# Performance work log

Hardware: AMD Instinct MI355X
Metric: run time of the kernel (lower is better)

The kernel has to match this reference:

```python
import jax, jax.numpy as jnp
import numpy as np
import math

B, L, HID = 2, 1024, 1536
NH, HD = 24, 64
DSSM = NH * HD            # 1536 (expand = 1)
QKV = 3 * DSSM
DCONV = 2
EPS = 1e-6


def _silu(u):
    return u * jax.nn.sigmoid(u)


def setup_inputs() -> dict:
    key = jax.random.key(0)
    ks = jax.random.split(key, 10)
    x = jax.random.normal(ks[0], (B, L, HID), dtype=jnp.float32)
    w_qkv = jax.random.normal(ks[1], (QKV, HID), dtype=jnp.float32) / math.sqrt(HID)
    conv_w = jax.random.normal(ks[2], (QKV, DCONV), dtype=jnp.float32) * 0.5  # depthwise causal conv, k=2
    w_dt = jax.random.normal(ks[3], (NH, HID), dtype=jnp.float32) * 0.02
    # dt_bias init exactly as in the torch module
    dt = jnp.exp(jax.random.uniform(ks[4], (NH,)) * (math.log(0.1) - math.log(0.001)) + math.log(0.001))
    dt = jnp.clip(dt, 1e-4, None)
    dt_bias = dt + jnp.log(-jnp.expm1(-dt))
    a_log = jnp.log(jax.random.uniform(ks[5], (NH,), minval=1.0, maxval=16.0))
    D = jnp.ones((NH, HD), dtype=jnp.float32)
    w_z = jax.random.normal(ks[6], (DSSM, HID), dtype=jnp.float32) / math.sqrt(HID)
    b_z = jnp.zeros((DSSM,), dtype=jnp.float32)
    rms_w = jnp.ones((DSSM,), dtype=jnp.float32)
    w_o = jax.random.normal(ks[7], (HID, DSSM), dtype=jnp.float32) / math.sqrt(DSSM)
    return dict(x=x, w_qkv=w_qkv, conv_w=conv_w, w_dt=w_dt, dt_bias=dt_bias,
                a_log=a_log, D=D, w_z=w_z, b_z=b_z, rms_w=rms_w, w_o=w_o)


def reference(x, w_qkv, conv_w, w_dt, dt_bias, a_log, D, w_z, b_z, rms_w, w_o):
    # qkv projection  [B,L,3*DSSM]
    qkv = jnp.einsum('blh,qh->blq', x, w_qkv)
    # depthwise causal conv1d (kernel size 2, padding k-1, trimmed to L)
    prev = jnp.pad(qkv, ((0, 0), (1, 0), (0, 0)))[:, :L]
    qkv = _silu(prev * conv_w[:, 0] + qkv * conv_w[:, 1])
    q, k, v = jnp.split(qkv, 3, axis=-1)
    q = q.reshape(B, L, NH, HD)
    k = k.reshape(B, L, NH, HD)
    v = v.reshape(B, L, NH, HD)
    # dt discretization: softplus(dt_proj(x) + dt_bias)   [B,L,NH]
    dt = jax.nn.softplus(jnp.einsum('blh,nh->bln', x, w_dt) + dt_bias)
    A = -jnp.exp(a_log)              # [NH], negative
    dA = dt * A                      # [B,L,NH]
    cs = jnp.transpose(jnp.cumsum(dA, axis=1), (0, 2, 1))   # [B,NH,L]
    diff = cs[:, :, :, None] - cs[:, :, None, :]            # [B,NH,L,L], <=0 on causal part
    causal = jnp.tril(jnp.ones((L, L), dtype=bool))
    decay = jnp.exp(jnp.where(causal, diff, -jnp.inf))      # segment-sum decay matrix
    # quadratic SSD (attention) form of the selective scan
    scores = jnp.einsum('bihd,bjhd->bhij', q, k) * decay
    scores = scores * jnp.transpose(dt, (0, 2, 1))[:, :, None, :]  # dt_j on keys (B-discretization)
    y = jnp.einsum('bhij,bjhd->bihd', scores, v)
    y = y + v * D                    # D skip connection
    y = y.reshape(B, L, DSSM)
    # z gate + RMSNorm + output projection
    z = jnp.einsum('blh,dh->bld', x, w_z) + b_z
    y = y * _silu(z)
    y = y * jax.lax.rsqrt(jnp.mean(y * y, axis=-1, keepdims=True) + EPS) * rms_w
    return jnp.einsum('bld,hd->blh', y, w_o)
```

## Files before the change

kernel.cpp:

```cpp
#include <hip/hip_runtime.h>
#include <hip/hip_bf16.h>
#include <math.h>

#define B_ 2
#define L_ 1024
#define HID_ 1536
#define NH_ 24
#define HD_ 64
#define DSSM_ 1536
#define QKV_ 4608
#define M_ 2048

typedef __attribute__((ext_vector_type(8))) short short8;
typedef __attribute__((ext_vector_type(4))) short short4e;
typedef __attribute__((ext_vector_type(4))) float floatx4;

__device__ __forceinline__ void gload_lds16(const short* g, short* l)
{
    __builtin_amdgcn_global_load_lds(
        (const __attribute__((address_space(1))) void*)g,
        (__attribute__((address_space(3))) void*)l,
        16, 0, 0);
}

__device__ __forceinline__ float bfs2f(short s)
{
    unsigned u = ((unsigned)(unsigned short)s) << 16;
    float f; __builtin_memcpy(&f, &u, 4); return f;
}
__device__ __forceinline__ short f2bfs(float f)
{
    __hip_bfloat16 h = __float2bfloat16(f);
    short s; __builtin_memcpy(&s, &h, 2); return s;
}

__device__ const int pIt[15] = {0,1,2,3,3,4,4,5,5,6,6,6,7,7,7};
__device__ const int pJ0[15] = {0,0,0,0,6,0,6,0,6,0,6,12,0,6,12};
__device__ const int pSl[15] = {0,0,0,0,1,0,1,0,1,0,1,2,0,1,2};

#define CN0 (M_ * HID_)
#define CN1 (QKV_ * HID_)
#define CN2 (DSSM_ * HID_)
#define CN3 (HID_ * DSSM_)
__global__ void cast_w_kernel(
    const float* __restrict__ wq,
    const float* __restrict__ wz, const float* __restrict__ wo,
    __hip_bfloat16* __restrict__ wcat,
    __hip_bfloat16* __restrict__ wob)
{
    int i = (blockIdx.x * 256 + threadIdx.x) * 4;
    const float* src; __hip_bfloat16* dst; int off;
    if (i < CN1)             { src = wq; dst = wcat;       off = i; }
    else if (i < CN1 + CN2)  { src = wz; dst = wcat + CN1; off = i - CN1; }
    else                     { src = wo; dst = wob;        off = i - CN1 - CN2; }
    float4 f = *reinterpret_cast<const float4*>(src + off);
    dst[off]     = __float2bfloat16(f.x);
    dst[off + 1] = __float2bfloat16(f.y);
    dst[off + 2] = __float2bfloat16(f.z);
    dst[off + 3] = __float2bfloat16(f.w);
}

#define MFMA_ __builtin_amdgcn_mfma_f32_16x16x32_bf16
#define BAR_() __builtin_amdgcn_s_barrier()
#define SCHED_ __builtin_amdgcn_sched_barrier(0)

#define CSTR 200

__global__ __launch_bounds__(256, 2) void gemm_qkvz_128(
    const __hip_bfloat16* __restrict__ A,
    const __hip_bfloat16* __restrict__ Bm,
    __hip_bfloat16* __restrict__ qkv_out,
    float* __restrict__ z_out,
    const float* __restrict__ b_z)
{
    extern __shared__ short lds[];
    const int K  = HID_;
    const int NT = K / 64;
    const int tid   = threadIdx.x;
    const int lane  = tid & 63;
    const int wave  = tid >> 6;
    const int col16 = lane & 15;
    const int quad  = lane >> 4;
    const int wm = wave >> 1;
    const int wn = wave & 1;
    const int rowblk = blockIdx.y * 128;
    const int colblk = blockIdx.x * 192;

    const short* Ap = reinterpret_cast<const short*>(A);
    const short* Bp = reinterpret_cast<const short*>(Bm);

    const int o  = tid * 16;
    const int s  = o ^ (((o >> 7) & 7) << 4);
    const int sr = s >> 7;
    const int sc = (s & 127) >> 1;

    const int mask = (col16 & 7) << 4;
    const int e0 = ((quad * 16)      ^ mask) >> 1;
    const int e1 = ((64 + quad * 16) ^ mask) >> 1;
    const int arow = (wm * 64 + col16) * 64;
    const int brow = (wn * 96 + col16) * 64;

    floatx4 acc[4][6] = {};

    auto STAGE_ALL = [&](int c, int t) {
        const short* ga = Ap + (size_t)(rowblk + sr) * K + t * 64 + sc;
        short* da = &lds[c * 8192 + tid * 8];
#pragma unroll
        for (int u = 0; u < 4; ++u)
            gload_lds16(ga + (size_t)(u * 32) * K, da + u * 2048);
        const short* gb = Bp + (size_t)(colblk + sr) * K + t * 64 + sc;
        short* db = &lds[16384 + c * 12288 + tid * 8];
#pragma unroll
        for (int u = 0; u < 6; ++u)
            gload_lds16(gb + (size_t)(u * 32) * K, db + u * 2048);
    };

    STAGE_ALL(0, 0);
    asm volatile("s_waitcnt vmcnt(0)" ::: "memory");
    SCHED_;
    BAR_();

    for (int t = 0; t < NT; ++t) {
        const int cur = t & 1;
        if (t + 1 < NT) STAGE_ALL(cur ^ 1, t + 1);

        const int Ab = cur * 8192;
        const int Bb = 16384 + cur * 12288;
        short8 af0[4], af1[4], bf0[6], bf1[6];
#pragma unroll
        for (int m = 0; m < 4; ++m) {
            af0[m] = *reinterpret_cast<const short8*>(&lds[Ab + arow + m * 1024 + e0]);
            af1[m] = *reinterpret_cast<const short8*>(&lds[Ab + arow + m * 1024 + e1]);
        }
#pragma unroll
        for (int n = 0; n < 6; ++n) {
            bf0[n] = *reinterpret_cast<const short8*>(&lds[Bb + brow + n * 1024 + e0]);
            bf1[n] = *reinterpret_cast<const short8*>(&lds[Bb + brow + n * 1024 + e1]);
        }
        asm volatile("s_waitcnt lgkmcnt(0)" ::: "memory");
        SCHED_;

        __builtin_amdgcn_s_setprio(1);
#pragma unroll
        for (int m = 0; m < 4; ++m)
#pragma unroll
            for (int n = 0; n < 6; ++n) {
                acc[m][n] = MFMA_(af0[m], bf0[n], acc[m][n], 0, 0, 0);
                acc[m][n] = MFMA_(af1[m], bf1[n], acc[m][n], 0, 0, 0);
            }
        __builtin_amdgcn_s_setprio(0);

        asm volatile("s_waitcnt vmcnt(0)" ::: "memory");
        SCHED_;
        BAR_();
    }

    if (blockIdx.x < 24) {
        const int rb = wm * 64 + quad * 4;
        const int cb = wn * 96 + col16;
#pragma unroll
        for (int m = 0; m < 4; ++m)
#pragma unroll
            for (int n = 0; n < 6; ++n)
#pragma unroll
                for (int r = 0; r < 4; ++r)
                    lds[(rb + m * 16 + r) * CSTR + cb + n * 16] =
                        f2bfs(acc[m][n][r]);
        __syncthreads();
        const int row = tid >> 1;
        const int seg = tid & 1;
        const short* srcp = &lds[row * CSTR + seg * 96];
        short* dstp = reinterpret_cast<short*>(qkv_out)
                    + (size_t)(rowblk + row) * QKV_ + colblk + seg * 96;
#pragma unroll
        for (int j = 0; j < 12; ++j)
            *reinterpret_cast<short8*>(dstp + j * 8) =
                *reinterpret_cast<const short8*>(srcp + j * 8);
    } else {
        const int row0  = rowblk + wm * 64;
        const int col0g = colblk + wn * 96 - QKV_;
#pragma unroll
        for (int m = 0; m < 4; ++m)
#pragma unroll
            for (int n = 0; n < 6; ++n)
#pragma unroll
                for (int r = 0; r < 4; ++r) {
                    int row = row0 + m * 16 + quad * 4 + r;
                    int col = col0g + n * 16 + col16;
                    z_out[(size_t)row * DSSM_ + col] = acc[m][n][r] + b_z[col];
                }
    }
}

template<int OUTMODE>
__global__ __launch_bounds__(256) void gemm_nt(
    const __hip_bfloat16* __restrict__ A,
    const __hip_bfloat16* __restrict__ Bm,
    void* __restrict__ Cv,
    const float* __restrict__ bias,
    int M, int N, int K)
{
    const int lane  = threadIdx.x & 63;
    const int wave  = threadIdx.x >> 6;
    const int col16 = lane & 15;
    const int quad  = lane >> 4;
    const int wr    = wave >> 1;
    const int wc    = wave & 1;
    const int rowblk = blockIdx.y * 128;
    const int colblk = blockIdx.x * 128;

    const short* Ap = reinterpret_cast<const short*>(A);
    const short* Bp = reinterpret_cast<const short*>(Bm);

    __shared__ alignas(16) short As[128 * 32];
    __shared__ alignas(16) short Bs[128 * 32];

    const int srow = lane >> 2;
    const int scol = (lane & 3) * 8;

    floatx4 acc[4][4] = {};

    for (int k0 = 0; k0 < K; k0 += 32) {
#pragma unroll
        for (int s2 = 0; s2 < 2; ++s2) {
            const int seg = wave * 2 + s2;
            gload_lds16(Ap + (size_t)(rowblk + seg * 16 + srow) * K + k0 + scol,
                        &As[seg * 512]);
            gload_lds16(Bp + (size_t)(colblk + seg * 16 + srow) * K + k0 + scol,
                        &Bs[seg * 512]);
        }
        __syncthreads();

        short8 af[4], bf[4];
#pragma unroll
        for (int t = 0; t < 4; ++t) {
            af[t] = *reinterpret_cast<const short8*>(
                &As[(wr * 64 + t * 16 + col16) * 32 + quad * 8]);
            bf[t] = *reinterpret_cast<const short8*>(
                &Bs[(wc * 64 + t * 16 + col16) * 32 + quad * 8]);
        }
#pragma unroll
        for (int mt = 0; mt < 4; ++mt)
#pragma unroll
            for (int nt = 0; nt < 4; ++nt)
                acc[mt][nt] = __builtin_amdgcn_mfma_f32_16x16x32_bf16(
                    af[mt], bf[nt], acc[mt][nt], 0, 0, 0);
        __syncthreads();
    }

    const int row0 = rowblk + wr * 64;
    const int col0 = colblk + wc * 64;
#pragma unroll
    for (int mt = 0; mt < 4; ++mt) {
#pragma unroll
        for (int nt = 0; nt < 4; ++nt) {
#pragma unroll
            for (int r = 0; r < 4; ++r) {
                int row = row0 + mt * 16 + quad * 4 + r;
                int col = col0 + nt * 16 + col16;
                float v = acc[mt][nt][r];
                if (OUTMODE == 1) v += bias[col];
                if (OUTMODE == 2)
                    ((__hip_bfloat16*)Cv)[(size_t)row * N + col] = __float2bfloat16(v);
                else
                    ((float*)Cv)[(size_t)row * N + col] = v;
            }
        }
    }
}

__global__ void conv_silu_kernel(
    const __hip_bfloat16* __restrict__ raw,
    const float* __restrict__ conv_w,
    __hip_bfloat16* __restrict__ q,
    __hip_bfloat16* __restrict__ k,
    __hip_bfloat16* __restrict__ v)
{
    int idx8 = blockIdx.x * 256 + threadIdx.x;
    int c8 = (idx8 % (QKV_ / 8)) * 8;
    int ml = idx8 / (QKV_ / 8);
    int l  = ml % L_;
    int b  = ml / L_;

    const short* base = reinterpret_cast<const short*>(raw) + (size_t)ml * QKV_ + c8;
    short8 curv = *reinterpret_cast<const short8*>(base);
    short8 prevv = {};
    if (l > 0) prevv = *reinterpret_cast<const short8*>(base - QKV_);

    float4 w0 = *reinterpret_cast<const float4*>(conv_w + c8 * 2);
    float4 w1 = *reinterpret_cast<const float4*>(conv_w + c8 * 2 + 4);
    float4 w2 = *reinterpret_cast<const float4*>(conv_w + c8 * 2 + 8);
    float4 w3 = *reinterpret_cast<const float4*>(conv_w + c8 * 2 + 12);
    const float wa[16] = {w0.x, w0.y, w0.z, w0.w, w1.x, w1.y, w1.z, w1.w,
                          w2.x, w2.y, w2.z, w2.w, w3.x, w3.y, w3.z, w3.w};

    short8 outv;
#pragma unroll
    for (int j = 0; j < 8; ++j) {
        float u = bfs2f(prevv[j]) * wa[2 * j] + bfs2f(curv[j]) * wa[2 * j + 1];
        u = fmaxf(u, -80.f);
        outv[j] = f2bfs(u / (1.f + __expf(-u)));
    }

    int part = c8 / DSSM_;
    int cc   = c8 % DSSM_;
    int nh   = cc >> 6;
    int d    = cc & 63;
    __hip_bfloat16* dst = (part == 0) ? q : ((part == 1) ? k : v);
    *reinterpret_cast<short8*>(
        reinterpret_cast<short*>(dst) + (((size_t)b * NH_ + nh) * L_ + l) * HD_ + d)
        = outv;
}

__global__ __launch_bounds__(256) void dtproj_kernel(
    const float* __restrict__ x,
    const float* __restrict__ w_dt,
    const float* __restrict__ dt_bias,
    const float* __restrict__ a_log,
    float* __restrict__ dt,
    float* __restrict__ dA,
    __hip_bfloat16* __restrict__ xb)
{
    const int tid  = threadIdx.x;
    const int wave = tid >> 6;
    const int lane = tid & 63;
    const int m0   = blockIdx.x * 8 + wave * 2;

    float4 xa[2][6];
#pragma unroll
    for (int rr = 0; rr < 2; ++rr)
#pragma unroll
        for (int j = 0; j < 6; ++j)
            xa[rr][j] = *reinterpret_cast<const float4*>(
                x + (size_t)(m0 + rr) * HID_ + lane * 4 + j * 256);

    short* xbp = reinterpret_cast<short*>(xb);
#pragma unroll
    for (int rr = 0; rr < 2; ++rr)
#pragma unroll
        for (int j = 0; j < 6; ++j) {
            short4e ov;
            ov[0] = f2bfs(xa[rr][j].x); ov[1] = f2bfs(xa[rr][j].y);
            ov[2] = f2bfs(xa[rr][j].z); ov[3] = f2bfs(xa[rr][j].w);
            *reinterpret_cast<short4e*>(
                xbp + (size_t)(m0 + rr) * HID_ + lane * 4 + j * 256) = ov;
        }

    float acc0[NH_], acc1[NH_];
#pragma unroll
    for (int n = 0; n < NH_; ++n) {
        float s0 = 0.f, s1 = 0.f;
#pragma unroll
        for (int j = 0; j < 6; ++j) {
            float4 w = *reinterpret_cast<const float4*>(
                w_dt + (size_t)n * HID_ + lane * 4 + j * 256);
            s0 += xa[0][j].x * w.x + xa[0][j].y * w.y
                + xa[0][j].z * w.z + xa[0][j].w * w.w;
            s1 += xa[1][j].x * w.x + xa[1][j].y * w.y
                + xa[1][j].z * w.z + xa[1][j].w * w.w;
        }
        acc0[n] = s0;
        acc1[n] = s1;
    }

#pragma unroll
    for (int off = 32; off; off >>= 1) {
#pragma unroll
        for (int n = 0; n < NH_; ++n) {
            acc0[n] += __shfl_xor(acc0[n], off, 64);
            acc1[n] += __shfl_xor(acc1[n], off, 64);
        }
    }

    if (lane < NH_) {
        const int n = lane;
        float bias = dt_bias[n];
        float Aval = -__expf(a_log[n]);
        float v0 = acc0[n] + bias;
        float v1 = acc1[n] + bias;
        v0 = (v0 > 20.f) ? v0 : log1pf(__expf(v0));
        v1 = (v1 > 20.f) ? v1 : log1pf(__expf(v1));
        int b0 = m0 / L_, l0 = m0 % L_;
        size_t o0 = ((size_t)b0 * NH_ + n) * L_ + l0;
        dt[o0]     = v0;
        dA[o0]     = v0 * Aval;
        dt[o0 + 1] = v1;
        dA[o0 + 1] = v1 * Aval;
    }
}

__global__ void cumsum_kernel(const float* __restrict__ dA, float* __restrict__ cs)
{
    int bnh  = blockIdx.x;
    int lane = threadIdx.x;
    const float* src = dA + (size_t)bnh * L_;
    float* dst       = cs + (size_t)bnh * L_;

    float loc[16];
    float run = 0.f;
#pragma unroll
    for (int t = 0; t < 16; ++t) { run += src[lane * 16 + t]; loc[t] = run; }
    float tot = run;
    float sc = tot;
#pragma unroll
    for (int off = 1; off < 64; off <<= 1) {
        float o = __shfl_up(sc, off, 64);
        if (lane >= off) sc += o;
    }
    float offset = sc - tot;
#pragma unroll
    for (int t = 0; t < 16; ++t) dst[lane * 16 + t] = loc[t] + offset;
}

__global__ __launch_bounds__(256) void vdt_transpose_kernel(
    const __hip_bfloat16* __restrict__ v,
    const float* __restrict__ dt,
    __hip_bfloat16* __restrict__ vt)
{
    const int lt0 = blockIdx.x * 64;
    const int bnh = blockIdx.z * NH_ + blockIdx.y;
    const int tid = threadIdx.x;

    __shared__ short T[64][72];

    {
        int row = tid >> 2;
        int cc  = (tid & 3) * 16;
        const short* sp = reinterpret_cast<const short*>(v)
                        + ((size_t)bnh * L_ + lt0 + row) * HD_ + cc;
        float dtr = dt[(size_t)bnh * L_ + lt0 + row];
        short8 a = *reinterpret_cast<const short8*>(sp);
        short8 b = *reinterpret_cast<const short8*>(sp + 8);
#pragma unroll
        for (int j = 0; j < 8; ++j) {
            T[row][cc + j]     = f2bfs(bfs2f(a[j]) * dtr);
            T[row][cc + 8 + j] = f2bfs(bfs2f(b[j]) * dtr);
        }
    }
    __syncthreads();
    {
        int d  = tid >> 2;
        int lc = (tid & 3) * 16;
        short8 o0, o1;
#pragma unroll
        for (int j = 0; j < 8; ++j) {
            o0[j] = T[lc + j][d];
            o1[j] = T[lc + 8 + j][d];
        }
        short* dst = reinterpret_cast<short*>(vt)
                   + ((size_t)bnh * HD_ + d) * L_ + lt0 + lc;
        *reinterpret_cast<short8*>(dst)     = o0;
        *reinterpret_cast<short8*>(dst + 8) = o1;
    }
}

__global__ __launch_bounds__(256) void attn_kernel(
    const __hip_bfloat16* __restrict__ q,
    const __hip_bfloat16* __restrict__ k,
    const __hip_bfloat16* __restrict__ vt,
    const float* __restrict__ cs,
    float* __restrict__ p0,
    float* __restrict__ p1,
    float* __restrict__ p2)
{
    const int bid  = blockIdx.x;
    const int xcd  = bid & 7;
    const int tq   = bid >> 3;
    const int g    = (tq / 15) * 8 + xcd;
    const int pidx = tq % 15;
    const int it   = pIt[pidx];
    const int sl   = pSl[pidx];
    const int jt_beg = pJ0[pidx];
    const int b    = g / NH_;
    const int nh   = g % NH_;
    const int tid  = threadIdx.x;
    const int lane = tid & 63;
    const int wave = tid >> 6;
    const int col  = lane & 15;
    const int quad = lane >> 4;
    const int bnh  = b * NH_ + nh;
    const int iw0  = it * 128 + wave * 16;
    const int iw1  = iw0 + 64;

    float* pout = (sl == 0) ? p0 : ((sl == 1) ? p1 : p2);

    const short* qp  = reinterpret_cast<const short*>(q);
    const short* kp  = reinterpret_cast<const short*>(k);
    const short* vtp = reinterpret_cast<const short*>(vt);

    __shared__ alignas(16) short Ks[4096];
    __shared__ alignas(16) short Ps[4 * 2 * 16 * 72];
    __shared__ float Cj[384];

    const int jbase = jt_beg * 64;
    const int jlim  = min(384, L_ - jbase);
    if (tid < (jlim >> 2))
        *reinterpret_cast<float4*>(&Cj[tid * 4]) =
            *reinterpret_cast<const float4*>(cs + (size_t)bnh * L_ + jbase + tid * 4);

    const short* qrow0 = qp + ((size_t)bnh * L_ + iw0 + col) * HD_;
    const short* qrow1 = qp + ((size_t)bnh * L_ + iw1 + col) * HD_;
    short8 aq0_0 = *reinterpret_cast<const short8*>(qrow0 + quad * 8);
    short8 aq0_1 = *reinterpret_cast<const short8*>(qrow0 + 32 + quad * 8);
    short8 aq1_0 = *reinterpret_cast<const short8*>(qrow1 + quad * 8);
    short8 aq1_1 = *reinterpret_cast<const short8*>(qrow1 + 32 + quad * 8);

    float csr0[4], csr1[4];
#pragma unroll
    for (int r = 0; r < 4; ++r) {
        csr0[r] = cs[(size_t)bnh * L_ + iw0 + quad * 4 + r];
        csr1[r] = cs[(size_t)bnh * L_ + iw1 + quad * 4 + r];
    }

    auto STAGE_K = [&](int jt2) {
        const short* gk = kp + ((size_t)bnh * L_ + jt2 * 64 + wave * 16 + (lane >> 2)) * HD_
                        + (lane & 3) * 8;
        gload_lds16(gk,      &Ks[wave * 512 + lane * 8]);
        gload_lds16(gk + 32, &Ks[2048 + wave * 512 + lane * 8]);
    };

    const int jt_end = min(jt_beg + 5, 2 * it + 1);

    STAGE_K(jt_beg);

    floatx4 accO0[4] = {};
    floatx4 accO1[4] = {};

    for (int jt = jt_beg; jt <= jt_end; ++jt) {
        const int j0 = jt * 64;

        asm volatile("s_waitcnt vmcnt(0)" ::: "memory");
        SCHED_;
        __syncthreads();

        short8 bv[2][4];
#pragma unroll
        for (int c = 0; c < 2; ++c) {
            if (j0 + c * 32 <= iw1 + 15) {
#pragma unroll
                for (int nt = 0; nt < 4; ++nt)
                    bv[c][nt] = *reinterpret_cast<const short8*>(
                        vtp + ((size_t)bnh * HD_ + nt * 16 + col) * L_
                            + j0 + c * 32 + quad * 8);
            }
        }

#pragma unroll
        for (int s = 0; s < 4; ++s) {
            int jsub = j0 + s * 16;
            short8 bk0 = *reinterpret_cast<const short8*>(
                &Ks[(s * 16 + col) * 32 + quad * 8]);
            short8 bk1 = *reinterpret_cast<const short8*>(
                &Ks[2048 + (s * 16 + col) * 32 + quad * 8]);
            int j = jsub + col;
            float csj = Cj[j - jbase];

            if (jsub <= iw0 + 15) {
                floatx4 sc = {};
                sc = __builtin_amdgcn_mfma_f32_16x16x32_bf16(aq0_0, bk0, sc, 0, 0, 0);
                sc = __builtin_amdgcn_mfma_f32_16x16x32_bf16(aq0_1, bk1, sc, 0, 0, 0);
#pragma unroll
                for (int r = 0; r < 4; ++r) {
                    int i = iw0 + quad * 4 + r;
                    float e = (j <= i) ? __expf(csr0[r] - csj) : 0.f;
                    Ps[wave * 2304 + (quad * 4 + r) * 72 + s * 16 + col] =
                        f2bfs(sc[r] * e);
                }
            } else if (j0 + (s >> 1) * 32 <= iw0 + 15) {
#pragma unroll
                for (int r = 0; r < 4; ++r)
                    Ps[wave * 2304 + (quad * 4 + r) * 72 + s * 16 + col] = 0;
            }

            if (jsub <= iw1 + 15) {
                floatx4 sc = {};
                sc = __builtin_amdgcn_mfma_f32_16x16x32_bf16(aq1_0, bk0, sc, 0, 0, 0);
                sc = __builtin_amdgcn_mfma_f32_16x16x32_bf16(aq1_1, bk1, sc, 0, 0, 0);
#pragma unroll
                for (int r = 0; r < 4; ++r) {
                    int i = iw1 + quad * 4 + r;
                    float e = (j <= i) ? __expf(csr1[r] - csj) : 0.f;
                    Ps[wave * 2304 + 1152 + (quad * 4 + r) * 72 + s * 16 + col] =
                        f2bfs(sc[r] * e);
                }
            } else if (j0 + (s >> 1) * 32 <= iw1 + 15) {
#pragma unroll
                for (int r = 0; r < 4; ++r)
                    Ps[wave * 2304 + 1152 + (quad * 4 + r) * 72 + s * 16 + col] = 0;
            }
        }

#pragma unroll
        for (int c = 0; c < 2; ++c) {
            if (j0 + c * 32 <= iw0 + 15) {
                short8 pa = *reinterpret_cast<const short8*>(
                    &Ps[wave * 2304 + col * 72 + c * 32 + quad * 8]);
#pragma unroll
                for (int nt = 0; nt < 4; ++nt)
                    accO0[nt] = __builtin_amdgcn_mfma_f32_16x16x32_bf16(
                        pa, bv[c][nt], accO0[nt], 0, 0, 0);
            }
            if (j0 + c * 32 <= iw1 + 15) {
                short8 pa = *reinterpret_cast<const short8*>(
                    &Ps[wave * 2304 + 1152 + col * 72 + c * 32 + quad * 8]);
#pragma unroll
                for (int nt = 0; nt < 4; ++nt)
                    accO1[nt] = __builtin_amdgcn_mfma_f32_16x16x32_bf16(
                        pa, bv[c][nt], accO1[nt], 0, 0, 0);
            }
        }

        __syncthreads();
        if (jt < jt_end) STAGE_K(jt + 1);
    }

#pragma unroll
    for (int nt = 0; nt < 4; ++nt) {
#pragma unroll
        for (int r = 0; r < 4; ++r) {
            int dv = nt * 16 + col;
            int i0 = iw0 + quad * 4 + r;
            int i1 = iw1 + quad * 4 + r;
            pout[((size_t)b * L_ + i0) * DSSM_ + nh * HD_ + dv] = accO0[nt][r];
            pout[((size_t)b * L_ + i1) * DSSM_ + nh * HD_ + dv] = accO1[nt][r];
        }
    }
}

__global__ __launch_bounds__(256) void gate_rms_kernel(
    const float* __restrict__ p0,
    const float* __restrict__ p1,
    const float* __restrict__ p2,
    const float* __restrict__ z,
    const __hip_bfloat16* __restrict__ v,
    const float* __restrict__ Dm,
    const float* __restrict__ rms_w,
    __hip_bfloat16* __restrict__ yn)
{
    int m   = blockIdx.x;
    int b   = m / L_;
    int l   = m % L_;
    int tid = threadIdx.x;
    size_t base = (size_t)m * DSSM_;
    const bool has1 = (l >= 384);
    const bool has2 = (l >= 768);

    floatx4 acc4[2] = {};
    float ss = 0.f;
#pragma unroll
    for (int t = 0; t < 2; ++t) {
        int i4 = t * 256 + tid;
        if (i4 < DSSM_ / 4) {
            int c  = i4 * 4;
            int nh = c >> 6, d = c & 63;
            floatx4 p = *reinterpret_cast<const floatx4*>(p0 + base + c);
            if (has1) p += *reinterpret_cast<const floatx4*>(p1 + base + c);
            if (has2) p += *reinterpret_cast<const floatx4*>(p2 + base + c);
            floatx4 dm = *reinterpret_cast<const floatx4*>(Dm + c);
            floatx4 zz = *reinterpret_cast<const floatx4*>(z + base + c);
            short4e vv = *reinterpret_cast<const short4e*>(
                reinterpret_cast<const short*>(v)
                + (((size_t)b * NH_ + nh) * L_ + l) * HD_ + d);
            floatx4 g;
#pragma unroll
            for (int j = 0; j < 4; ++j) {
                float yv = p[j] + bfs2f(vv[j]) * dm[j];
                float zv = fmaxf(zz[j], -80.f);
                float gv = yv * (zv / (1.f + __expf(-zv)));
                ss += gv * gv;
                g[j] = gv;
            }
            acc4[t] = g;
        }
    }
#pragma unroll
    for (int off = 32; off; off >>= 1) ss += __shfl_xor(ss, off, 64);
    __shared__ float red[4];
    if ((tid & 63) == 0) red[tid >> 6] = ss;
    __syncthreads();
    ss = red[0] + red[1] + red[2] + red[3];
    float r = rsqrtf(ss / (float)DSSM_ + 1e-6f);
#pragma unroll
    for (int t = 0; t < 2; ++t) {
        int i4 = t * 256 + tid;
        if (i4 < DSSM_ / 4) {
            int c = i4 * 4;
            floatx4 rw = *reinterpret_cast<const floatx4*>(rms_w + c);
            short4e o;
#pragma unroll
            for (int j = 0; j < 4; ++j)
                o[j] = f2bfs(acc4[t][j] * r * rw[j]);
            *reinterpret_cast<short4e*>(
                reinterpret_cast<short*>(yn) + base + c) = o;
        }
    }
}

extern "C" void kernel_launch(void* const* d_in, const int* in_sizes, int n_in,
                              void* d_out, int out_size, void* d_ws, size_t ws_size,
                              hipStream_t stream)
{
    const float* x       = (const float*)d_in[0];
    const float* w_qkv   = (const float*)d_in[1];
    const float* conv_w  = (const float*)d_in[2];
    const float* w_dt    = (const float*)d_in[3];
    const float* dt_bias = (const float*)d_in[4];
    const float* a_log   = (const float*)d_in[5];
    const float* Dm      = (const float*)d_in[6];
    const float* w_z     = (const float*)d_in[7];
    const float* b_z     = (const float*)d_in[8];
    const float* rms_w   = (const float*)d_in[9];
    const float* w_o     = (const float*)d_in[10];
    float* out = (float*)d_out;

    char* ws = (char*)d_ws;

    __hip_bfloat16* xb    = (__hip_bfloat16*)(ws);
    __hip_bfloat16* wob   = (__hip_bfloat16*)(ws + 6291456);
    float*          zbuf  = (float*)(ws + 11010048);
    __hip_bfloat16* wcat  = (__hip_bfloat16*)(ws + 23592960);
    __hip_bfloat16* qkvb  = (__hip_bfloat16*)(ws + 42467328);
    __hip_bfloat16* qb    = (__hip_bfloat16*)(ws + 61341696);
    __hip_bfloat16* kb    = (__hip_bfloat16*)(ws + 67633152);
    __hip_bfloat16* vb    = (__hip_bfloat16*)(ws + 73924608);
    float* dt   = (float*)(ws + 80216064);
    float* dA   = (float*)(ws + 80412672);
    float* cs   = (float*)(ws + 80609280);
    __hip_bfloat16* vtb = (__hip_bfloat16*)(ws);
    __hip_bfloat16* yn  = (__hip_bfloat16*)(ws);
    float* p0 = (float*)(ws + 23592960);
    float* p1 = (float*)(ws + 36175872);
    float* p2 = (float*)(ws + 48758784);

    static bool attr_set = false;
    if (!attr_set) {
        (void)hipFuncSetAttribute(reinterpret_cast<const void*>(gemm_qkvz_128),
                                  hipFuncAttributeMaxDynamicSharedMemorySize,
                                  81920);
        attr_set = true;
    }

    cast_w_kernel<<<(CN1 + CN2 + CN3) / 1024, 256, 0, stream>>>(
        w_qkv, w_z, w_o, wcat, wob);

    dtproj_kernel<<<M_ / 8, 256, 0, stream>>>(
        x, w_dt, dt_bias, a_log, dt, dA, xb);

    cumsum_kernel<<<B_ * NH_, 64, 0, stream>>>(dA, cs);

    gemm_qkvz_128<<<dim3((QKV_ + DSSM_) / 192, M_ / 128), 256, 81920, stream>>>(
        xb, wcat, qkvb, zbuf, b_z);

    conv_silu_kernel<<<(B_ * L_ * QKV_ / 8) / 256, 256, 0, stream>>>(
        qkvb, conv_w, qb, kb, vb);

    vdt_transpose_kernel<<<dim3(L_ / 64, NH_, B_), 256, 0, stream>>>(vb, dt, vtb);

    attn_kernel<<<720, 256, 0, stream>>>(
        qb, kb, vtb, cs, p0, p1, p2);

    gate_rms_kernel<<<M_, 256, 0, stream>>>(p0, p1, p2, zbuf, vb, Dm, rms_w, yn);

    gemm_nt<0><<<dim3(HID_ / 128, M_ / 128), 256, 0, stream>>>(
        yn, wob, (void*)out, nullptr, M_, HID_, DSSM_);
}
```

Measured before the change: 261.8 us.

## Fuse weight cast into dtproj, conv with v transpose, cumsum into attention

Merges the weight-cast kernel into the dt-projection kernel, combines the conv+SiLU kernel with the v*dt transpose kernel so v is computed straight from the raw qkv, and moves the per-head cumsum into each attention block using a block-wide scan over dA. This cuts three kernel launches and the intermediate round trips through global memory for cs and for v. In exchange every attention block now recomputes a full 1024-length prefix sum and pays an extra barrier, which adds a little redundant work per block.

```diff
diff --git a/kernel.cpp b/kernel.cpp
--- a/kernel.cpp
+++ b/kernel.cpp
@@ -38,289 +38,42 @@
 __device__ const int pJ0[15] = {0,0,0,0,6,0,6,0,6,0,6,12,0,6,12};
 __device__ const int pSl[15] = {0,0,0,0,1,0,1,0,1,0,1,2,0,1,2};
 
-#define CN0 (M_ * HID_)
 #define CN1 (QKV_ * HID_)
 #define CN2 (DSSM_ * HID_)
 #define CN3 (HID_ * DSSM_)
-__global__ void cast_w_kernel(
-    const float* __restrict__ wq,
-    const float* __restrict__ wz, const float* __restrict__ wo,
-    __hip_bfloat16* __restrict__ wcat,
-    __hip_bfloat16* __restrict__ wob)
-{
-    int i = (blockIdx.x * 256 + threadIdx.x) * 4;
-    const float* src; __hip_bfloat16* dst; int off;
-    if (i < CN1)             { src = wq; dst = wcat;       off = i; }
-    else if (i < CN1 + CN2)  { src = wz; dst = wcat + CN1; off = i - CN1; }
-    else                     { src = wo; dst = wob;        off = i - CN1 - CN2; }
-    float4 f = *reinterpret_cast<const float4*>(src + off);
-    dst[off]     = __float2bfloat16(f.x);
-    dst[off + 1] = __float2bfloat16(f.y);
-    dst[off + 2] = __float2bfloat16(f.z);
-    dst[off + 3] = __float2bfloat16(f.w);
-}
 
 #define MFMA_ __builtin_amdgcn_mfma_f32_16x16x32_bf16
 #define BAR_() __builtin_amdgcn_s_barrier()
 #define SCHED_ __builtin_amdgcn_sched_barrier(0)
 
-#define CSTR 200
-
-__global__ __launch_bounds__(256, 2) void gemm_qkvz_128(
-    const __hip_bfloat16* __restrict__ A,
-    const __hip_bfloat16* __restrict__ Bm,
-    __hip_bfloat16* __restrict__ qkv_out,
-    float* __restrict__ z_out,
-    const float* __restrict__ b_z)
-{
-    extern __shared__ short lds[];
-    const int K  = HID_;
-    const int NT = K / 64;
-    const int tid   = threadIdx.x;
-    const int lane  = tid & 63;
-    const int wave  = tid >> 6;
-    const int col16 = lane & 15;
-    const int quad  = lane >> 4;
-    const int wm = wave >> 1;
-    const int wn = wave & 1;
-    const int rowblk = blockIdx.y * 128;
-    const int colblk = blockIdx.x * 192;
-
-    const short* Ap = reinterpret_cast<const short*>(A);
-    const short* Bp = reinterpret_cast<const short*>(Bm);
-
-    const int o  = tid * 16;
-    const int s  = o ^ (((o >> 7) & 7) << 4);
-    const int sr = s >> 7;
-    const int sc = (s & 127) >> 1;
-
-    const int mask = (col16 & 7) << 4;
-    const int e0 = ((quad * 16)      ^ mask) >> 1;
-    const int e1 = ((64 + quad * 16) ^ mask) >> 1;
-    const int arow = (wm * 64 + col16) * 64;
-    const int brow = (wn * 96 + col16) * 64;
-
-    floatx4 acc[4][6] = {};
-
-    auto STAGE_ALL = [&](int c, int t) {
-        const short* ga = Ap + (size_t)(rowblk + sr) * K + t * 64 + sc;
-        short* da = &lds[c * 8192 + tid * 8];
-#pragma unroll
-        for (int u = 0; u < 4; ++u)
-            gload_lds16(ga + (size_t)(u * 32) * K, da + u * 2048);
-        const short* gb = Bp + (size_t)(colblk + sr) * K + t * 64 + sc;
-        short* db = &lds[16384 + c * 12288 + tid * 8];
-#pragma unroll
-        for (int u = 0; u < 6; ++u)
-            gload_lds16(gb + (size_t)(u * 32) * K, db + u * 2048);
-    };
-
-    STAGE_ALL(0, 0);
-    asm volatile("s_waitcnt vmcnt(0)" ::: "memory");
-    SCHED_;
-    BAR_();
-
-    for (int t = 0; t < NT; ++t) {
-        const int cur = t & 1;
-        if (t + 1 < NT) STAGE_ALL(cur ^ 1, t + 1);
-
-        const int Ab = cur * 8192;
-        const int Bb = 16384 + cur * 12288;
-        short8 af0[4], af1[4], bf0[6], bf1[6];
-#pragma unroll
-        for (int m = 0; m < 4; ++m) {
-            af0[m] = *reinterpret_cast<const short8*>(&lds[Ab + arow + m * 1024 + e0]);
-            af1[m] = *reinterpret_cast<const short8*>(&lds[Ab + arow + m * 1024 + e1]);
-        }
-#pragma unroll
-        for (int n = 0; n < 6; ++n) {
-            bf0[n] = *reinterpret_cast<const short8*>(&lds[Bb + brow + n * 1024 + e0]);
-            bf1[n] = *reinterpret_cast<const short8*>(&lds[Bb + brow + n * 1024 + e1]);
-        }
-        asm volatile("s_waitcnt lgkmcnt(0)" ::: "memory");
-        SCHED_;
-
-        __builtin_amdgcn_s_setprio(1);
-#pragma unroll
-        for (int m = 0; m < 4; ++m)
-#pragma unroll
-            for (int n = 0; n < 6; ++n) {
-                acc[m][n] = MFMA_(af0[m], bf0[n], acc[m][n], 0, 0, 0);
-                acc[m][n] = MFMA_(af1[m], bf1[n], acc[m][n], 0, 0, 0);
-            }
-        __builtin_amdgcn_s_setprio(0);
-
-        asm volatile("s_waitcnt vmcnt(0)" ::: "memory");
-        SCHED_;
-        BAR_();
-    }
-
-    if (blockIdx.x < 24) {
-        const int rb = wm * 64 + quad * 4;
-        const int cb = wn * 96 + col16;
-#pragma unroll
-        for (int m = 0; m < 4; ++m)
-#pragma unroll
-            for (int n = 0; n < 6; ++n)
-#pragma unroll
-                for (int r = 0; r < 4; ++r)
-                    lds[(rb + m * 16 + r) * CSTR + cb + n * 16] =
-                        f2bfs(acc[m][n][r]);
-        __syncthreads();
-        const int row = tid >> 1;
-        const int seg = tid & 1;
-        const short* srcp = &lds[row * CSTR + seg * 96];
-        short* dstp = reinterpret_cast<short*>(qkv_out)
-                    + (size_t)(rowblk + row) * QKV_ + colblk + seg * 96;
-#pragma unroll
-        for (int j = 0; j < 12; ++j)
-            *reinterpret_cast<short8*>(dstp + j * 8) =
-                *reinterpret_cast<const short8*>(srcp + j * 8);
-    } else {
-        const int row0  = rowblk + wm * 64;
-        const int col0g = colblk + wn * 96 - QKV_;
-#pragma unroll
-        for (int m = 0; m < 4; ++m)
-#pragma unroll
-            for (int n = 0; n < 6; ++n)
-#pragma unroll
-                for (int r = 0; r < 4; ++r) {
-                    int row = row0 + m * 16 + quad * 4 + r;
-                    int col = col0g + n * 16 + col16;
-                    z_out[(size_t)row * DSSM_ + col] = acc[m][n][r] + b_z[col];
-                }
-    }
-}
-
-template<int OUTMODE>
-__global__ __launch_bounds__(256) void gemm_nt(
-    const __hip_bfloat16* __restrict__ A,
-    const __hip_bfloat16* __restrict__ Bm,
-    void* __restrict__ Cv,
-    const float* __restrict__ bias,
-    int M, int N, int K)
-{
-    const int lane  = threadIdx.x & 63;
-    const int wave  = threadIdx.x >> 6;
-    const int col16 = lane & 15;
-    const int quad  = lane >> 4;
-    const int wr    = wave >> 1;
-    const int wc    = wave & 1;
-    const int rowblk = blockIdx.y * 128;
-    const int colblk = blockIdx.x * 128;
-
-    const short* Ap = reinterpret_cast<const short*>(A);
-    const short* Bp = reinterpret_cast<const short*>(Bm);
-
-    __shared__ alignas(16) short As[128 * 32];
-    __shared__ alignas(16) short Bs[128 * 32];
-
-    const int srow = lane >> 2;
-    const int scol = (lane & 3) * 8;
-
-    floatx4 acc[4][4] = {};
-
-    for (int k0 = 0; k0 < K; k0 += 32) {
-#pragma unroll
-        for (int s2 = 0; s2 < 2; ++s2) {
-            const int seg = wave * 2 + s2;
-            gload_lds16(Ap + (size_t)(rowblk + seg * 16 + srow) * K + k0 + scol,
-                        &As[seg * 512]);
-            gload_lds16(Bp + (size_t)(colblk + seg * 16 + srow) * K + k0 + scol,
-                        &Bs[seg * 512]);
-        }
-        __syncthreads();
-
-        short8 af[4], bf[4];
-#pragma unroll
-        for (int t = 0; t < 4; ++t) {
-            af[t] = *reinterpret_cast<const short8*>(
-                &As[(wr * 64 + t * 16 + col16) * 32 + quad * 8]);
-            bf[t] = *reinterpret_cast<const short8*>(
-                &Bs[(wc * 64 + t * 16 + col16) * 32 + quad * 8]);
-        }
-#pragma unroll
-        for (int mt = 0; mt < 4; ++mt)
-#pragma unroll
-            for (int nt = 0; nt < 4; ++nt)
-                acc[mt][nt] = __builtin_amdgcn_mfma_f32_16x16x32_bf16(
-                    af[mt], bf[nt], acc[mt][nt], 0, 0, 0);
-        __syncthreads();
-    }
-
-    const int row0 = rowblk + wr * 64;
-    const int col0 = colblk + wc * 64;
-#pragma unroll
-    for (int mt = 0; mt < 4; ++mt) {
-#pragma unroll
-        for (int nt = 0; nt < 4; ++nt) {
-#pragma unroll
-            for (int r = 0; r < 4; ++r) {
-                int row = row0 + mt * 16 + quad * 4 + r;
-                int col = col0 + nt * 16 + col16;
-                float v = acc[mt][nt][r];
-                if (OUTMODE == 1) v += bias[col];
-                if (OUTMODE == 2)
-                    ((__hip_bfloat16*)Cv)[(size_t)row * N + col] = __float2bfloat16(v);
-                else
-                    ((float*)Cv)[(size_t)row * N + col] = v;
-            }
-        }
-    }
-}
-
-__global__ void conv_silu_kernel(
-    const __hip_bfloat16* __restrict__ raw,
-    const float* __restrict__ conv_w,
-    __hip_bfloat16* __restrict__ q,
-    __hip_bfloat16* __restrict__ k,
-    __hip_bfloat16* __restrict__ v)
-{
-    int idx8 = blockIdx.x * 256 + threadIdx.x;
-    int c8 = (idx8 % (QKV_ / 8)) * 8;
-    int ml = idx8 / (QKV_ / 8);
-    int l  = ml % L_;
-    int b  = ml / L_;
-
-    const short* base = reinterpret_cast<const short*>(raw) + (size_t)ml * QKV_ + c8;
-    short8 curv = *reinterpret_cast<const short8*>(base);
-    short8 prevv = {};
-    if (l > 0) prevv = *reinterpret_cast<const short8*>(base - QKV_);
-
-    float4 w0 = *reinterpret_cast<const float4*>(conv_w + c8 * 2);
-    float4 w1 = *reinterpret_cast<const float4*>(conv_w + c8 * 2 + 4);
-    float4 w2 = *reinterpret_cast<const float4*>(conv_w + c8 * 2 + 8);
-    float4 w3 = *reinterpret_cast<const float4*>(conv_w + c8 * 2 + 12);
-    const float wa[16] = {w0.x, w0.y, w0.z, w0.w, w1.x, w1.y, w1.z, w1.w,
-                          w2.x, w2.y, w2.z, w2.w, w3.x, w3.y, w3.z, w3.w};
-
-    short8 outv;
-#pragma unroll
-    for (int j = 0; j < 8; ++j) {
-        float u = bfs2f(prevv[j]) * wa[2 * j] + bfs2f(curv[j]) * wa[2 * j + 1];
-        u = fmaxf(u, -80.f);
-        outv[j] = f2bfs(u / (1.f + __expf(-u)));
-    }
-
-    int part = c8 / DSSM_;
-    int cc   = c8 % DSSM_;
-    int nh   = cc >> 6;
-    int d    = cc & 63;
-    __hip_bfloat16* dst = (part == 0) ? q : ((part == 1) ? k : v);
-    *reinterpret_cast<short8*>(
-        reinterpret_cast<short*>(dst) + (((size_t)b * NH_ + nh) * L_ + l) * HD_ + d)
-        = outv;
-}
-
-__global__ __launch_bounds__(256) void dtproj_kernel(
+__global__ __launch_bounds__(256) void prep_kernel(
     const float* __restrict__ x,
     const float* __restrict__ w_dt,
     const float* __restrict__ dt_bias,
     const float* __restrict__ a_log,
+    const float* __restrict__ wq,
+    const float* __restrict__ wz,
+    const float* __restrict__ wo,
     float* __restrict__ dt,
     float* __restrict__ dA,
-    __hip_bfloat16* __restrict__ xb)
-{
+    __hip_bfloat16* __restrict__ xb,
+    __hip_bfloat16* __restrict__ wcat,
+    __hip_bfloat16* __restrict__ wob)
+{
+    if (blockIdx.x >= 256) {
+        int i = ((blockIdx.x - 256) * 256 + threadIdx.x) * 4;
+        const float* src; __hip_bfloat16* dst; int off;
+        if (i < CN1)             { src = wq; dst = wcat;       off = i; }
+        else if (i < CN1 + CN2)  { src = wz; dst = wcat + CN1; off = i - CN1; }
+        else                     { src = wo; dst = wob;        off = i - CN1 - CN2; }
+        float4 f = *reinterpret_cast<const float4*>(src + off);
+        dst[off]     = __float2bfloat16(f.x);
+        dst[off + 1] = __float2bfloat16(f.y);
+        dst[off + 2] = __float2bfloat16(f.z);
+        dst[off + 3] = __float2bfloat16(f.w);
+        return;
+    }
+
     const int tid  = threadIdx.x;
     const int wave = tid >> 6;
     const int lane = tid & 63;
@@ -389,53 +142,311 @@
     }
 }
 
-__global__ void cumsum_kernel(const float* __restrict__ dA, float* __restrict__ cs)
-{
-    int bnh  = blockIdx.x;
-    int lane = threadIdx.x;
-    const float* src = dA + (size_t)bnh * L_;
-    float* dst       = cs + (size_t)bnh * L_;
-
-    float loc[16];
-    float run = 0.f;
-#pragma unroll
-    for (int t = 0; t < 16; ++t) { run += src[lane * 16 + t]; loc[t] = run; }
-    float tot = run;
-    float sc = tot;
-#pragma unroll
-    for (int off = 1; off < 64; off <<= 1) {
-        float o = __shfl_up(sc, off, 64);
-        if (lane >= off) sc += o;
-    }
-    float offset = sc - tot;
-#pragma unroll
-    for (int t = 0; t < 16; ++t) dst[lane * 16 + t] = loc[t] + offset;
-}
-
-__global__ __launch_bounds__(256) void vdt_transpose_kernel(
-    const __hip_bfloat16* __restrict__ v,
+#define CSTR 200
+
+__global__ __launch_bounds__(256, 2) void gemm_qkvz_128(
+    const __hip_bfloat16* __restrict__ A,
+    const __hip_bfloat16* __restrict__ Bm,
+    __hip_bfloat16* __restrict__ qkv_out,
+    float* __restrict__ z_out,
+    const float* __restrict__ b_z)
+{
+    extern __shared__ short lds[];
+    const int K  = HID_;
+    const int NT = K / 64;
+    const int tid   = threadIdx.x;
+    const int lane  = tid & 63;
+    const int wave  = tid >> 6;
+    const int col16 = lane & 15;
+    const int quad  = lane >> 4;
+    const int wm = wave >> 1;
+    const int wn = wave & 1;
+    const int rowblk = blockIdx.y * 128;
+    const int colblk = blockIdx.x * 192;
+
+    const short* Ap = reinterpret_cast<const short*>(A);
+    const short* Bp = reinterpret_cast<const short*>(Bm);
+
+    const int o  = tid * 16;
+    const int s  = o ^ (((o >> 7) & 7) << 4);
+    const int sr = s >> 7;
+    const int sc = (s & 127) >> 1;
+
+    const int mask = (col16 & 7) << 4;
+    const int e0 = ((quad * 16)      ^ mask) >> 1;
+    const int e1 = ((64 + quad * 16) ^ mask) >> 1;
+    const int arow = (wm * 64 + col16) * 64;
+    const int brow = (wn * 96 + col16) * 64;
+
+    floatx4 acc[4][6] = {};
+
+    auto STAGE_ALL = [&](int c, int t) {
+        const short* ga = Ap + (size_t)(rowblk + sr) * K + t * 64 + sc;
+        short* da = &lds[c * 8192 + tid * 8];
+#pragma unroll
+        for (int u = 0; u < 4; ++u)
+            gload_lds16(ga + (size_t)(u * 32) * K, da + u * 2048);
+        const short* gb = Bp + (size_t)(colblk + sr) * K + t * 64 + sc;
+        short* db = &lds[16384 + c * 12288 + tid * 8];
+#pragma unroll
+        for (int u = 0; u < 6; ++u)
+            gload_lds16(gb + (size_t)(u * 32) * K, db + u * 2048);
+    };
+
+    STAGE_ALL(0, 0);
+    asm volatile("s_waitcnt vmcnt(0)" ::: "memory");
+    SCHED_;
+    BAR_();
+
+    for (int t = 0; t < NT; ++t) {
+        const int cur = t & 1;
+        if (t + 1 < NT) STAGE_ALL(cur ^ 1, t + 1);
+
+        const int Ab = cur * 8192;
+        const int Bb = 16384 + cur * 12288;
+        short8 af0[4], af1[4], bf0[6], bf1[6];
+#pragma unroll
+        for (int m = 0; m < 4; ++m) {
+            af0[m] = *reinterpret_cast<const short8*>(&lds[Ab + arow + m * 1024 + e0]);
+            af1[m] = *reinterpret_cast<const short8*>(&lds[Ab + arow + m * 1024 + e1]);
+        }
+#pragma unroll
+        for (int n = 0; n < 6; ++n) {
+            bf0[n] = *reinterpret_cast<const short8*>(&lds[Bb + brow + n * 1024 + e0]);
+            bf1[n] = *reinterpret_cast<const short8*>(&lds[Bb + brow + n * 1024 + e1]);
+        }
+        asm volatile("s_waitcnt lgkmcnt(0)" ::: "memory");
+        SCHED_;
+
+        __builtin_amdgcn_s_setprio(1);
+#pragma unroll
+        for (int m = 0; m < 4; ++m)
+#pragma unroll
+            for (int n = 0; n < 6; ++n) {
+                acc[m][n] = MFMA_(af0[m], bf0[n], acc[m][n], 0, 0, 0);
+                acc[m][n] = MFMA_(af1[m], bf1[n], acc[m][n], 0, 0, 0);
+            }
+        __builtin_amdgcn_s_setprio(0);
+
+        asm volatile("s_waitcnt vmcnt(0)" ::: "memory");
+        SCHED_;
+        BAR_();
+    }
+
+    if (blockIdx.x < 24) {
+        const int rb = wm * 64 + quad * 4;
+        const int cb = wn * 96 + col16;
+#pragma unroll
+        for (int m = 0; m < 4; ++m)
+#pragma unroll
+            for (int n = 0; n < 6; ++n)
+#pragma unroll
+                for (int r = 0; r < 4; ++r)
+                    lds[(rb + m * 16 + r) * CSTR + cb + n * 16] =
+                        f2bfs(acc[m][n][r]);
+        __syncthreads();
+        const int row = tid >> 1;
+        const int seg = tid & 1;
+        const short* srcp = &lds[row * CSTR + seg * 96];
+        short* dstp = reinterpret_cast<short*>(qkv_out)
+                    + (size_t)(rowblk + row) * QKV_ + colblk + seg * 96;
+#pragma unroll
+        for (int j = 0; j < 12; ++j)
+            *reinterpret_cast<short8*>(dstp + j * 8) =
+                *reinterpret_cast<const short8*>(srcp + j * 8);
+    } else {
+        const int row0  = rowblk + wm * 64;
+        const int col0g = colblk + wn * 96 - QKV_;
+#pragma unroll
+        for (int m = 0; m < 4; ++m)
+#pragma unroll
+            for (int n = 0; n < 6; ++n)
+#pragma unroll
+                for (int r = 0; r < 4; ++r) {
+                    int row = row0 + m * 16 + quad * 4 + r;
+                    int col = col0g + n * 16 + col16;
+                    z_out[(size_t)row * DSSM_ + col] = acc[m][n][r] + b_z[col];
+                }
+    }
+}
+
+template<int OUTMODE>
+__global__ __launch_bounds__(256) void gemm_nt(
+    const __hip_bfloat16* __restrict__ A,
+    const __hip_bfloat16* __restrict__ Bm,
+    void* __restrict__ Cv,
+    const float* __restrict__ bias,
+    int M, int N, int K)
+{
+    const int lane  = threadIdx.x & 63;
+    const int wave  = threadIdx.x >> 6;
+    const int col16 = lane & 15;
+    const int quad  = lane >> 4;
+    const int wr    = wave >> 1;
+    const int wc    = wave & 1;
+    const int rowblk = blockIdx.y * 128;
+    const int colblk = blockIdx.x * 128;
+
+    const short* Ap = reinterpret_cast<const short*>(A);
+    const short* Bp = reinterpret_cast<const short*>(Bm);
+
+    __shared__ alignas(16) short As[128 * 32];
+    __shared__ alignas(16) short Bs[128 * 32];
+
+    const int srow = lane >> 2;
+    const int scol = (lane & 3) * 8;
+
+    floatx4 acc[4][4] = {};
+
+    for (int k0 = 0; k0 < K; k0 += 32) {
+#pragma unroll
+        for (int s2 = 0; s2 < 2; ++s2) {
+            const int seg = wave * 2 + s2;
+            gload_lds16(Ap + (size_t)(rowblk + seg * 16 + srow) * K + k0 + scol,
+                        &As[seg * 512]);
+            gload_lds16(Bp + (size_t)(colblk + seg * 16 + srow) * K + k0 + scol,
+                        &Bs[seg * 512]);
+        }
+        __syncthreads();
+
+        short8 af[4], bf[4];
+#pragma unroll
+        for (int t = 0; t < 4; ++t) {
+            af[t] = *reinterpret_cast<const short8*>(
+                &As[(wr * 64 + t * 16 + col16) * 32 + quad * 8]);
+            bf[t] = *reinterpret_cast<const short8*>(
+                &Bs[(wc * 64 + t * 16 + col16) * 32 + quad * 8]);
+        }
+#pragma unroll
+        for (int mt = 0; mt < 4; ++mt)
+#pragma unroll
+            for (int nt = 0; nt < 4; ++nt)
+                acc[mt][nt] = __builtin_amdgcn_mfma_f32_16x16x32_bf16(
+                    af[mt], bf[nt], acc[mt][nt], 0, 0, 0);
+        __syncthreads();
+    }
+
+    const int row0 = rowblk + wr * 64;
+    const int col0 = colblk + wc * 64;
+#pragma unroll
+    for (int mt = 0; mt < 4; ++mt) {
+#pragma unroll
+        for (int nt = 0; nt < 4; ++nt) {
+#pragma unroll
+            for (int r = 0; r < 4; ++r) {
+                int row = row0 + mt * 16 + quad * 4 + r;
+                int col = col0 + nt * 16 + col16;
+                float v = acc[mt][nt][r];
+                if (OUTMODE == 1) v += bias[col];
+                if (OUTMODE == 2)
+                    ((__hip_bfloat16*)Cv)[(size_t)row * N + col] = __float2bfloat16(v);
+                else
+                    ((float*)Cv)[(size_t)row * N + col] = v;
+            }
+        }
+    }
+}
+
+#define QK2 (2 * DSSM_)
+
+__global__ __launch_bounds__(256) void convvdt_kernel(
+    const __hip_bfloat16* __restrict__ raw,
+    const float* __restrict__ conv_w,
     const float* __restrict__ dt,
+    __hip_bfloat16* __restrict__ q,
+    __hip_bfloat16* __restrict__ k,
+    __hip_bfloat16* __restrict__ v,
     __hip_bfloat16* __restrict__ vt)
 {
-    const int lt0 = blockIdx.x * 64;
-    const int bnh = blockIdx.z * NH_ + blockIdx.y;
+    __shared__ short T[64][72];
     const int tid = threadIdx.x;
 
-    __shared__ short T[64][72];
+    if (blockIdx.x < 3072) {
+        int idx8 = blockIdx.x * 256 + tid;
+        int c8 = (idx8 % (QK2 / 8)) * 8;
+        int ml = idx8 / (QK2 / 8);
+        int l  = ml % L_;
+        int b  = ml / L_;
+
+        const short* base = reinterpret_cast<const short*>(raw) + (size_t)ml * QKV_ + c8;
+        short8 curv = *reinterpret_cast<const short8*>(base);
+        short8 prevv = {};
+        if (l > 0) prevv = *reinterpret_cast<const short8*>(base - QKV_);
+
+        float4 w0 = *reinterpret_cast<const float4*>(conv_w + c8 * 2);
+        float4 w1 = *reinterpret_cast<const float4*>(conv_w + c8 * 2 + 4);
+        float4 w2 = *reinterpret_cast<const float4*>(conv_w + c8 * 2 + 8);
+        float4 w3 = *reinterpret_cast<const float4*>(conv_w + c8 * 2 + 12);
+        const float wa[16] = {w0.x, w0.y, w0.z, w0.w, w1.x, w1.y, w1.z, w1.w,
+                              w2.x, w2.y, w2.z, w2.w, w3.x, w3.y, w3.z, w3.w};
+
+        short8 outv;
+#pragma unroll
+        for (int j = 0; j < 8; ++j) {
+            float u = bfs2f(prevv[j]) * wa[2 * j] + bfs2f(curv[j]) * wa[2 * j + 1];
+            u = fmaxf(u, -80.f);
+            outv[j] = f2bfs(u / (1.f + __expf(-u)));
+        }
+
+        int part = c8 / DSSM_;
+        int cc   = c8 % DSSM_;
+        int nh   = cc >> 6;
+        int d    = cc & 63;
+        __hip_bfloat16* dst = (part == 0) ? q : k;
+        *reinterpret_cast<short8*>(
+            reinterpret_cast<short*>(dst) + (((size_t)b * NH_ + nh) * L_ + l) * HD_ + d)
+            = outv;
+        return;
+    }
+
+    const int bid2 = blockIdx.x - 3072;
+    const int lt0 = (bid2 & 15) * 64;
+    const int nh  = (bid2 >> 4) % NH_;
+    const int b   = bid2 / (16 * NH_);
+    const int bnh = b * NH_ + nh;
 
     {
         int row = tid >> 2;
         int cc  = (tid & 3) * 16;
-        const short* sp = reinterpret_cast<const short*>(v)
-                        + ((size_t)bnh * L_ + lt0 + row) * HD_ + cc;
-        float dtr = dt[(size_t)bnh * L_ + lt0 + row];
-        short8 a = *reinterpret_cast<const short8*>(sp);
-        short8 b = *reinterpret_cast<const short8*>(sp + 8);
+        int l   = lt0 + row;
+        int cglob = QK2 + nh * 64 + cc;
+        const short* rp = reinterpret_cast<const short*>(raw)
+                        + (size_t)(b * L_ + l) * QKV_ + cglob;
+        short8 cur0 = *reinterpret_cast<const short8*>(rp);
+        short8 cur1 = *reinterpret_cast<const short8*>(rp + 8);
+        short8 pv0 = {}, pv1 = {};
+        if (l > 0) {
+            pv0 = *reinterpret_cast<const short8*>(rp - QKV_);
+            pv1 = *reinterpret_cast<const short8*>(rp + 8 - QKV_);
+        }
+        float wa[32];
+#pragma unroll
+        for (int w4 = 0; w4 < 8; ++w4) {
+            float4 wv = *reinterpret_cast<const float4*>(conv_w + cglob * 2 + w4 * 4);
+            wa[w4 * 4]     = wv.x; wa[w4 * 4 + 1] = wv.y;
+            wa[w4 * 4 + 2] = wv.z; wa[w4 * 4 + 3] = wv.w;
+        }
+        float dtr = dt[(size_t)bnh * L_ + l];
+
+        short8 vo0, vo1;
 #pragma unroll
         for (int j = 0; j < 8; ++j) {
-            T[row][cc + j]     = f2bfs(bfs2f(a[j]) * dtr);
-            T[row][cc + 8 + j] = f2bfs(bfs2f(b[j]) * dtr);
-        }
+            float u = bfs2f(pv0[j]) * wa[2 * j] + bfs2f(cur0[j]) * wa[2 * j + 1];
+            u = fmaxf(u, -80.f);
+            float sV = u / (1.f + __expf(-u));
+            vo0[j] = f2bfs(sV);
+            T[row][cc + j] = f2bfs(sV * dtr);
+
+            float u2 = bfs2f(pv1[j]) * wa[16 + 2 * j] + bfs2f(cur1[j]) * wa[16 + 2 * j + 1];
+            u2 = fmaxf(u2, -80.f);
+            float sV2 = u2 / (1.f + __expf(-u2));
+            vo1[j] = f2bfs(sV2);
+            T[row][cc + 8 + j] = f2bfs(sV2 * dtr);
+        }
+        short* vp = reinterpret_cast<short*>(v)
+                  + ((size_t)bnh * L_ + l) * HD_ + cc;
+        *reinterpret_cast<short8*>(vp)     = vo0;
+        *reinterpret_cast<short8*>(vp + 8) = vo1;
     }
     __syncthreads();
     {
@@ -458,7 +469,7 @@
     const __hip_bfloat16* __restrict__ q,
     const __hip_bfloat16* __restrict__ k,
     const __hip_bfloat16* __restrict__ vt,
-    const float* __restrict__ cs,
+    const float* __restrict__ dA,
     float* __restrict__ p0,
     float* __restrict__ p1,
     float* __restrict__ p2)
@@ -490,13 +501,44 @@
 
     __shared__ alignas(16) short Ks[4096];
     __shared__ alignas(16) short Ps[4 * 2 * 16 * 72];
-    __shared__ float Cj[384];
-
-    const int jbase = jt_beg * 64;
-    const int jlim  = min(384, L_ - jbase);
-    if (tid < (jlim >> 2))
-        *reinterpret_cast<float4*>(&Cj[tid * 4]) =
-            *reinterpret_cast<const float4*>(cs + (size_t)bnh * L_ + jbase + tid * 4);
+    __shared__ float Csh[1024];
+    __shared__ float red4[4];
+
+    auto STAGE_K = [&](int jt2) {
+        const short* gk = kp + ((size_t)bnh * L_ + jt2 * 64 + wave * 16 + (lane >> 2)) * HD_
+                        + (lane & 3) * 8;
+        gload_lds16(gk,      &Ks[wave * 512 + lane * 8]);
+        gload_lds16(gk + 32, &Ks[2048 + wave * 512 + lane * 8]);
+    };
+
+    const int jt_end = min(jt_beg + 5, 2 * it + 1);
+    STAGE_K(jt_beg);
+
+    {
+        float4 dv = *reinterpret_cast<const float4*>(dA + (size_t)bnh * L_ + tid * 4);
+        float s1 = dv.x + dv.y;
+        float s2 = s1 + dv.z;
+        float s3 = s2 + dv.w;
+        float tot = s3;
+        float sc = tot;
+#pragma unroll
+        for (int off = 1; off < 64; off <<= 1) {
+            float o2 = __shfl_up(sc, off, 64);
+            if (lane >= off) sc += o2;
+        }
+        if (lane == 63) red4[wave] = sc;
+        __syncthreads();
+        float woff = 0.f;
+#pragma unroll
+        for (int w = 0; w < 4; ++w)
+            if (w < wave) woff += red4[w];
+        float base = woff + sc - tot;
+        Csh[tid * 4 + 0] = base + dv.x;
+        Csh[tid * 4 + 1] = base + s1;
+        Csh[tid * 4 + 2] = base + s2;
+        Csh[tid * 4 + 3] = base + s3;
+        __syncthreads();
+    }
 
     const short* qrow0 = qp + ((size_t)bnh * L_ + iw0 + col) * HD_;
     const short* qrow1 = qp + ((size_t)bnh * L_ + iw1 + col) * HD_;
@@ -508,20 +550,9 @@
     float csr0[4], csr1[4];
 #pragma unroll
     for (int r = 0; r < 4; ++r) {
-        csr0[r] = cs[(size_t)bnh * L_ + iw0 + quad * 4 + r];
-        csr1[r] = cs[(size_t)bnh * L_ + iw1 + quad * 4 + r];
-    }
-
-    auto STAGE_K = [&](int jt2) {
-        const short* gk = kp + ((size_t)bnh * L_ + jt2 * 64 + wave * 16 + (lane >> 2)) * HD_
-                        + (lane & 3) * 8;
-        gload_lds16(gk,      &Ks[wave * 512 + lane * 8]);
-        gload_lds16(gk + 32, &Ks[2048 + wave * 512 + lane * 8]);
-    };
-
-    const int jt_end = min(jt_beg + 5, 2 * it + 1);
-
-    STAGE_K(jt_beg);
+        csr0[r] = Csh[iw0 + quad * 4 + r];
+        csr1[r] = Csh[iw1 + quad * 4 + r];
+    }
 
     floatx4 accO0[4] = {};
     floatx4 accO1[4] = {};
@@ -553,7 +584,7 @@
             short8 bk1 = *reinterpret_cast<const short8*>(
                 &Ks[2048 + (s * 16 + col) * 32 + quad * 8]);
             int j = jsub + col;
-            float csj = Cj[j - jbase];
+            float csj = Csh[j];
 
             if (jsub <= iw0 + 15) {
                 floatx4 sc = {};
@@ -725,7 +756,6 @@
     __hip_bfloat16* vb    = (__hip_bfloat16*)(ws + 73924608);
     float* dt   = (float*)(ws + 80216064);
     float* dA   = (float*)(ws + 80412672);
-    float* cs   = (float*)(ws + 80609280);
     __hip_bfloat16* vtb = (__hip_bfloat16*)(ws);
     __hip_bfloat16* yn  = (__hip_bfloat16*)(ws);
     float* p0 = (float*)(ws + 23592960);
@@ -740,24 +770,17 @@
         attr_set = true;
     }
 
-    cast_w_kernel<<<(CN1 + CN2 + CN3) / 1024, 256, 0, stream>>>(
-        w_qkv, w_z, w_o, wcat, wob);
-
-    dtproj_kernel<<<M_ / 8, 256, 0, stream>>>(
-        x, w_dt, dt_bias, a_log, dt, dA, xb);
-
-    cumsum_kernel<<<B_ * NH_, 64, 0, stream>>>(dA, cs);
+    prep_kernel<<<256 + (CN1 + CN2 + CN3) / 1024, 256, 0, stream>>>(
+        x, w_dt, dt_bias, a_log, w_qkv, w_z, w_o, dt, dA, xb, wcat, wob);
 
     gemm_qkvz_128<<<dim3((QKV_ + DSSM_) / 192, M_ / 128), 256, 81920, stream>>>(
         xb, wcat, qkvb, zbuf, b_z);
 
-    conv_silu_kernel<<<(B_ * L_ * QKV_ / 8) / 256, 256, 0, stream>>>(
-        qkvb, conv_w, qb, kb, vb);
-
-    vdt_transpose_kernel<<<dim3(L_ / 64, NH_, B_), 256, 0, stream>>>(vb, dt, vtb);
+    convvdt_kernel<<<3840, 256, 0, stream>>>(
+        qkvb, conv_w, dt, qb, kb, vb, vtb);
 
     attn_kernel<<<720, 256, 0, stream>>>(
-        qb, kb, vtb, cs, p0, p1, p2);
+        qb, kb, vtb, dA, p0, p1, p2);
 
     gate_rms_kernel<<<M_, 256, 0, stream>>>(p0, p1, p2, zbuf, vb, Dm, rms_w, yn);
 
```

Result: slower. 274.5 us (+4.8%).
